# Optimization experiments

Hardware: AMD Instinct MI355X
Metric: run time of the kernel (lower is better)

Reference implementation:

```python
import jax, jax.numpy as jnp
import numpy as np

N = 50000       # nodes
E = 800000      # edges (avg degree 16)
R = 8           # relations
IN = 128        # in_channels
H = 128         # hidden_size
B = 10          # graphs in batch
NPG = N // B    # nodes per graph (equal-size graphs)
NEG_SLOPE = 0.2 # RGATConv default negative_slope


def setup_inputs() -> dict:
    key = jax.random.key(0)
    ks = jax.random.split(key, 12)
    s = 0.1
    x = jax.random.normal(ks[0], (N, IN), dtype=jnp.float32)
    edge_index = jax.random.randint(ks[1], (2, E), 0, N, dtype=jnp.int32)
    edge_type = jax.random.randint(ks[2], (E,), 0, R, dtype=jnp.int32)
    batch = jnp.repeat(jnp.arange(B, dtype=jnp.int32), NPG)
    W1 = jax.random.normal(ks[3], (R, IN, H), dtype=jnp.float32) * s
    q1 = jax.random.normal(ks[4], (H, 1), dtype=jnp.float32) * s
    k1 = jax.random.normal(ks[5], (H, 1), dtype=jnp.float32) * s
    b1 = jnp.zeros((H,), dtype=jnp.float32)
    W2 = jax.random.normal(ks[6], (R, H, H), dtype=jnp.float32) * s
    q2 = jax.random.normal(ks[7], (H, 1), dtype=jnp.float32) * s
    k2 = jax.random.normal(ks[8], (H, 1), dtype=jnp.float32) * s
    b2 = jnp.zeros((H,), dtype=jnp.float32)
    Wl = jax.random.normal(ks[9], (H, H), dtype=jnp.float32) * s
    bl = jnp.zeros((H,), dtype=jnp.float32)
    return dict(x=x, edge_index=edge_index, edge_type=edge_type, batch=batch,
                W1=W1, q1=q1, k1=k1, b1=b1, W2=W2, q2=q2, k2=k2, b2=b2,
                Wl=Wl, bl=bl)


def _rgat_conv(x, src, tgt, etype, W, q, k, b):
    # Per-relation transform once per node ([R,N,H]), then gather per edge;
    # mathematically identical to PyG's per-edge bmm but avoids the [E,in,H] blowup.
    xW = jnp.einsum('ni,rio->rno', x, W)          # [R, N, H]
    outi = xW[etype, tgt]                          # [E, H] transformed target feats
    outj = xW[etype, src]                          # [E, H] transformed source feats
    # additive self-attention, heads=1, dim=1
    alpha = jax.nn.leaky_relu(outi @ q + outj @ k, NEG_SLOPE)  # [E, 1]
    # across-relation segment softmax over incoming edges of each target node
    m = jax.ops.segment_max(alpha, tgt, num_segments=N)        # [N, 1]
    a = jnp.exp(alpha - m[tgt])
    den = jax.ops.segment_sum(a, tgt, num_segments=N)          # [N, 1]
    a = a / (den[tgt] + 1e-16)
    out = jax.ops.segment_sum(a * outj, tgt, num_segments=N)   # [N, H]
    return out + b


def reference(x, edge_index, edge_type, batch, W1, q1, k1, b1,
              W2, q2, k2, b2, Wl, bl):
    src, tgt = edge_index[0], edge_index[1]
    h = jax.nn.relu(_rgat_conv(x, src, tgt, edge_type, W1, q1, k1, b1))
    # dropout p=0 -> identity
    h = jax.nn.relu(_rgat_conv(h, src, tgt, edge_type, W2, q2, k2, b2))
    h = h @ Wl.T + bl                               # nn.Linear
    # to_dense_batch: batch is sorted with equal-size graphs of NPG nodes
    return h.reshape(B, NPG, H)
```

## Files before the change

### kernel.cpp

```cpp
#include <hip/hip_runtime.h>


typedef unsigned int uint;
typedef unsigned short ushort_t;

using bf16x8 = __attribute__((ext_vector_type(8))) __bf16;
using f32x4  = __attribute__((ext_vector_type(4))) float;

__device__ __forceinline__ ushort_t fToBf(float f) {
  uint u = __float_as_uint(f);
  u += 0x7FFFu + ((u >> 16) & 1);
  return (ushort_t)(u >> 16);
}
__device__ __forceinline__ float bfToF(ushort_t h) {
  return __uint_as_float(((uint)h) << 16);
}
__device__ __forceinline__ uint packBf(float a, float b) {
  return (uint)fToBf(a) | ((uint)fToBf(b) << 16);
}


__global__ void k_count(const int* __restrict__ tgt, int* __restrict__ deg, int E) {
  int e = blockIdx.x * 256 + threadIdx.x;
  if (e < E) atomicAdd(&deg[tgt[e]], 1);
}

__global__ void k_scanA(const int* __restrict__ deg, int* __restrict__ incl,
                        int* __restrict__ bsum, int n) {
  __shared__ int s[256];
  int tid = threadIdx.x;
  int i = blockIdx.x * 256 + tid;
  int v = (i < n) ? deg[i] : 0;
  s[tid] = v;
  __syncthreads();
  for (int off = 1; off < 256; off <<= 1) {
    int t = (tid >= off) ? s[tid - off] : 0;
    __syncthreads();
    s[tid] += t;
    __syncthreads();
  }
  if (i < n) incl[i] = s[tid];
  if (tid == 255) bsum[blockIdx.x] = s[255];
}

__global__ void k_scanB(int* __restrict__ bsum, int nb) {
  __shared__ int s[256];
  int tid = threadIdx.x;
  int v = (tid < nb) ? bsum[tid] : 0;
  s[tid] = v;
  __syncthreads();
  for (int off = 1; off < 256; off <<= 1) {
    int t = (tid >= off) ? s[tid - off] : 0;
    __syncthreads();
    s[tid] += t;
    __syncthreads();
  }
  if (tid < nb) bsum[tid] = s[tid] - v;
}

__global__ void k_scanC(const int* __restrict__ deg, const int* __restrict__ incl,
                        const int* __restrict__ bsum, int* __restrict__ rowptr,
                        int n, int E) {
  int i = blockIdx.x * 256 + threadIdx.x;
  if (i < n) {
    rowptr[i] = bsum[blockIdx.x] + incl[i] - deg[i];
    if (i == n - 1) rowptr[n] = E;
  }
}

__global__ void k_scatter(const int* __restrict__ src, const int* __restrict__ tgt,
                          const int* __restrict__ et, const int* __restrict__ rowptr,
                          int* __restrict__ cursor, int* __restrict__ sorted, int E) {
  int e = blockIdx.x * 256 + threadIdx.x;
  if (e >= E) return;
  int t = tgt[e];
  int pos = atomicAdd(&cursor[t], 1);
  sorted[rowptr[t] + pos] = src[e] | (et[e] << 16);
}


__global__ void k_wTf(const float* __restrict__ W1, const float* __restrict__ W2,
                      ushort_t* __restrict__ WTf) {
  int b = blockIdx.x * 4 + (threadIdx.x >> 6);
  int lane = threadIdx.x & 63;
  int layer = b >> 8;
  int r = (b >> 5) & 7;
  int f = b & 31;
  int mt = f >> 2, kb = f & 3;
  const float* W = layer ? W2 : W1;
  int col = mt * 16 + (lane & 15);
  int krow = kb * 32 + (lane >> 4) * 8;
  ushort_t* dst = WTf + ((size_t)b * 64 + lane) * 8;
  #pragma unroll
  for (int j = 0; j < 8; j++)
    dst[j] = fToBf(W[((size_t)r * 128 + krow + j) * 128 + col]);
}

__global__ void k_wqwk(const float* __restrict__ W1, const float* __restrict__ q1,
                       const float* __restrict__ k1, const float* __restrict__ W2,
                       const float* __restrict__ q2, const float* __restrict__ k2,
                       ushort_t* __restrict__ wqk) {
  int g = blockIdx.x * 256 + threadIdx.x;
  if (g >= 4096) return;
  int layer = g >> 11;
  int which = (g >> 10) & 1;
  int idx = g & 1023;
  const float* w = (layer ? W2 : W1) + (size_t)idx * 128;
  const float* v = layer ? (which ? k2 : q2) : (which ? k1 : q1);
  float s = 0.f;
  #pragma unroll 8
  for (int h = 0; h < 128; h++) s += w[h] * v[h];
  int r = idx >> 7, kin = idx & 127;
  wqk[(size_t)layer * 2048 + ((which << 3) + r) * 128 + kin] = fToBf(s);
}


template <bool F32IN>
__global__ __launch_bounds__(256, 2) void
k_xw(const void* __restrict__ Ain,
     const ushort_t* __restrict__ WTf,
     const ushort_t* __restrict__ Wqk,
     ushort_t* __restrict__ xW,
     float* __restrict__ stbl,
     int M) {
  __shared__ __align__(16) ushort_t wbuf[2][16384];
  int tid = threadIdx.x, wv = tid >> 6, lane = tid & 63;
  int l15 = lane & 15, quad = lane >> 4;
  int node0 = blockIdx.x * 128 + wv * 32;

  bf16x8 bx[2][4];
  #pragma unroll
  for (int tile = 0; tile < 2; tile++) {
    int node = node0 + tile * 16 + l15;
    int nc = node < M ? node : M - 1;
    if (F32IN) {
      const float* row = (const float*)Ain + (size_t)nc * 128;
      #pragma unroll
      for (int kb = 0; kb < 4; kb++) {
        float4 a = *(const float4*)(row + kb * 32 + quad * 8);
        float4 b = *(const float4*)(row + kb * 32 + quad * 8 + 4);
        union { bf16x8 v; ushort_t u[8]; } t;
        t.u[0] = fToBf(a.x); t.u[1] = fToBf(a.y); t.u[2] = fToBf(a.z); t.u[3] = fToBf(a.w);
        t.u[4] = fToBf(b.x); t.u[5] = fToBf(b.y); t.u[6] = fToBf(b.z); t.u[7] = fToBf(b.w);
        bx[tile][kb] = t.v;
      }
    } else {
      const ushort_t* row = (const ushort_t*)Ain + (size_t)nc * 128;
      #pragma unroll
      for (int kb = 0; kb < 4; kb++)
        bx[tile][kb] = *(const bf16x8*)(row + kb * 32 + quad * 8);
    }
  }

  #pragma unroll
  for (int i = 0; i < 8; i++)
    *(int4*)(wbuf[0] + (size_t)(tid + i * 256) * 8) =
        *(const int4*)(WTf + (size_t)(tid + i * 256) * 8);
  __syncthreads();

  for (int r = 0; r < 8; r++) {
    int4 pf[8];
    if (r < 7) {
      const ushort_t* src = WTf + (size_t)(r + 1) * 16384;
      #pragma unroll
      for (int i = 0; i < 8; i++)
        pf[i] = *(const int4*)(src + (size_t)(tid + i * 256) * 8);
    }
    const ushort_t* wb = wbuf[r & 1];
    uint2 po[2][8];
    #pragma unroll
    for (int mt = 0; mt < 8; mt++) {
      f32x4 a0 = {}, a1 = {};
      #pragma unroll
      for (int kb = 0; kb < 4; kb++) {
        bf16x8 af = *(const bf16x8*)(wb + (size_t)((mt * 4 + kb) * 64 + lane) * 8);
        a0 = __builtin_amdgcn_mfma_f32_16x16x32_bf16(af, bx[0][kb], a0, 0, 0, 0);
        a1 = __builtin_amdgcn_mfma_f32_16x16x32_bf16(af, bx[1][kb], a1, 0, 0, 0);
      }
      po[0][mt].x = packBf(a0[0], a0[1]); po[0][mt].y = packBf(a0[2], a0[3]);
      po[1][mt].x = packBf(a1[0], a1[1]); po[1][mt].y = packBf(a1[2], a1[3]);
    }
    #pragma unroll
    for (int tile = 0; tile < 2; tile++) {
      int node = node0 + tile * 16 + l15;
      if (node < M) {
        ushort_t* rowp = xW + ((size_t)r * M + node) * 128 + quad * 32;
        #pragma unroll
        for (int i = 0; i < 4; i++) {
          int4 v = {(int)po[tile][2 * i].x, (int)po[tile][2 * i].y,
                    (int)po[tile][2 * i + 1].x, (int)po[tile][2 * i + 1].y};
          *(int4*)(rowp + i * 8) = v;
        }
      }
    }
    if (r < 7) {
      ushort_t* db = wbuf[(r + 1) & 1];
      #pragma unroll
      for (int i = 0; i < 8; i++)
        *(int4*)(db + (size_t)(tid + i * 256) * 8) = pf[i];
    }
    __syncthreads();
  }

  bf16x8 aq[4];
  #pragma unroll
  for (int kb = 0; kb < 4; kb++)
    aq[kb] = *(const bf16x8*)(Wqk + (size_t)l15 * 128 + kb * 32 + quad * 8);
  #pragma unroll
  for (int tile = 0; tile < 2; tile++) {
    f32x4 s = {};
    #pragma unroll
    for (int kb = 0; kb < 4; kb++)
      s = __builtin_amdgcn_mfma_f32_16x16x32_bf16(aq[kb], bx[tile][kb], s, 0, 0, 0);
    int node = node0 + tile * 16 + l15;
    if (node < M) {
      float4 v = {s[0], s[1], s[2], s[3]};
      *(float4*)(stbl + (size_t)node * 16 + quad * 4) = v;
    }
  }
}


#define ACC8(W_, V_)                                                     \
  acc[0] += W_ * bfToF((ushort_t)(V_.x & 0xFFFF));                       \
  acc[1] += W_ * bfToF((ushort_t)(V_.x >> 16));                          \
  acc[2] += W_ * bfToF((ushort_t)(V_.y & 0xFFFF));                       \
  acc[3] += W_ * bfToF((ushort_t)(V_.y >> 16));                          \
  acc[4] += W_ * bfToF((ushort_t)(V_.z & 0xFFFF));                       \
  acc[5] += W_ * bfToF((ushort_t)(V_.z >> 16));                          \
  acc[6] += W_ * bfToF((ushort_t)(V_.w & 0xFFFF));                       \
  acc[7] += W_ * bfToF((ushort_t)(V_.w >> 16));

__global__ __launch_bounds__(256) void
k_aggr(const ushort_t* __restrict__ feat,
       const float* __restrict__ stbl,
       const int* __restrict__ rowptr, const int* __restrict__ sorted,
       const float* __restrict__ bias, ushort_t* __restrict__ outp, int n) {
  int tid = threadIdx.x, wv = tid >> 6, lane = tid & 63;
  int t = blockIdx.x * 4 + wv;
  if (t >= n) return;
  int e0 = rowptr[t], e1 = rowptr[t + 1];
  int g4 = lane >> 4, fcol = lane & 15;

  float m = -INFINITY, den = 0.f;
  float acc[8] = {};

  for (int base = e0; base < e1; base += 64) {
    int cnt = min(64, e1 - base);
    float alpha = -INFINITY;
    int pk = 0;
    if (lane < cnt) {
      pk = sorted[base + lane];
      int s = pk & 0xFFFF, r = pk >> 16;
      float a = stbl[(size_t)t * 16 + r] + stbl[(size_t)s * 16 + 8 + r];
      alpha = (a >= 0.f) ? a : 0.2f * a;
    }
    float cm = alpha;
    #pragma unroll
    for (int off = 32; off; off >>= 1) cm = fmaxf(cm, __shfl_xor(cm, off, 64));
    float nm = fmaxf(m, cm);
    float sc = __expf(m - nm);
    den *= sc;
    #pragma unroll
    for (int i = 0; i < 8; i++) acc[i] *= sc;
    float w = (lane < cnt) ? __expf(alpha - nm) : 0.f;
    float ws = w;
    #pragma unroll
    for (int off = 32; off; off >>= 1) ws += __shfl_xor(ws, off, 64);
    den += ws;
    m = nm;

    for (int g = 0; g < cnt; g += 16) {
      int i0 = g + g4;
      float w0 = __shfl(w, i0, 64);
      float w1 = __shfl(w, i0 + 4, 64);
      float w2 = __shfl(w, i0 + 8, 64);
      float w3 = __shfl(w, i0 + 12, 64);
      int p0 = __shfl(pk, i0, 64);
      int p1 = __shfl(pk, i0 + 4, 64);
      int p2 = __shfl(pk, i0 + 8, 64);
      int p3 = __shfl(pk, i0 + 12, 64);
      const uint4* r0 = (const uint4*)(feat + (size_t)((p0 >> 16) * n + (p0 & 0xFFFF)) * 128) + fcol;
      const uint4* r1 = (const uint4*)(feat + (size_t)((p1 >> 16) * n + (p1 & 0xFFFF)) * 128) + fcol;
      const uint4* r2 = (const uint4*)(feat + (size_t)((p2 >> 16) * n + (p2 & 0xFFFF)) * 128) + fcol;
      const uint4* r3 = (const uint4*)(feat + (size_t)((p3 >> 16) * n + (p3 & 0xFFFF)) * 128) + fcol;
      uint4 v0 = *r0;
      uint4 v1 = *r1;
      uint4 v2 = *r2;
      uint4 v3 = *r3;
      ACC8(w0, v0)
      ACC8(w1, v1)
      ACC8(w2, v2)
      ACC8(w3, v3)
    }
  }

  #pragma unroll
  for (int i = 0; i < 8; i++) acc[i] += __shfl_xor(acc[i], 16, 64);
  #pragma unroll
  for (int i = 0; i < 8; i++) acc[i] += __shfl_xor(acc[i], 32, 64);

  float inv = (den > 0.f) ? 1.f / (den + 1e-16f) : 0.f;
  int base0 = (fcol & 3) * 32 + (fcol >> 2) * 4;
  float4 ba = *(const float4*)(bias + base0);
  float4 bb = *(const float4*)(bias + base0 + 16);
  uint2 oa, ob;
  oa.x = packBf(fmaxf(acc[0] * inv + ba.x, 0.f), fmaxf(acc[1] * inv + ba.y, 0.f));
  oa.y = packBf(fmaxf(acc[2] * inv + ba.z, 0.f), fmaxf(acc[3] * inv + ba.w, 0.f));
  ob.x = packBf(fmaxf(acc[4] * inv + bb.x, 0.f), fmaxf(acc[5] * inv + bb.y, 0.f));
  ob.y = packBf(fmaxf(acc[6] * inv + bb.z, 0.f), fmaxf(acc[7] * inv + bb.w, 0.f));
  if (lane < 16) {
    *(uint2*)(outp + (size_t)t * 128 + base0) = oa;
    *(uint2*)(outp + (size_t)t * 128 + base0 + 16) = ob;
  }
}


#define LDA 136

__global__ __launch_bounds__(256) void
k_gemmL(const ushort_t* __restrict__ A, const float* __restrict__ Wl,
        float* __restrict__ Cout, const float* __restrict__ bias, int M) {
  __shared__ ushort_t As[64 * LDA];
  __shared__ ushort_t Bs[128 * LDA];
  int tid = threadIdx.x;
  int row0 = blockIdx.x * 64;
  for (int c = tid; c < 1024; c += 256) {
    int r = c >> 4, off = (c & 15) * 8;
    int4 v = {0, 0, 0, 0};
    if (row0 + r < M) v = *(const int4*)(A + (size_t)(row0 + r) * 128 + off);
    *(int4*)(As + r * LDA + off) = v;
  }
  for (int c = tid; c < 2048; c += 256) {
    int nn = c >> 4, off = (c & 15) * 8;
    float4 a = *(const float4*)(Wl + (size_t)nn * 128 + off);
    float4 b = *(const float4*)(Wl + (size_t)nn * 128 + off + 4);
    ushort_t* d = Bs + nn * LDA + off;
    d[0] = fToBf(a.x); d[1] = fToBf(a.y); d[2] = fToBf(a.z); d[3] = fToBf(a.w);
    d[4] = fToBf(b.x); d[5] = fToBf(b.y); d[6] = fToBf(b.z); d[7] = fToBf(b.w);
  }
  __syncthreads();
  int wv = tid >> 6, lane = tid & 63;
  int l15 = lane & 15, quad = lane >> 4;
  int wr = wv * 16;
  bf16x8 afr[4];
  #pragma unroll
  for (int kb = 0; kb < 4; kb++)
    afr[kb] = *reinterpret_cast<const bf16x8*>(As + (wr + l15) * LDA + kb * 32 + quad * 8);
  f32x4 acc[8] = {};
  #pragma unroll
  for (int ct = 0; ct < 8; ct++)
    #pragma unroll
    for (int kb = 0; kb < 4; kb++) {
      bf16x8 bfr = *reinterpret_cast<const bf16x8*>(Bs + (ct * 16 + l15) * LDA + kb * 32 + quad * 8);
      acc[ct] = __builtin_amdgcn_mfma_f32_16x16x32_bf16(afr[kb], bfr, acc[ct], 0, 0, 0);
    }
  #pragma unroll
  for (int ct = 0; ct < 8; ct++)
    #pragma unroll
    for (int reg = 0; reg < 4; reg++) {
      int rr = row0 + wr + quad * 4 + reg;
      if (rr < M) Cout[(size_t)rr * 128 + ct * 16 + l15] = acc[ct][reg] + bias[ct * 16 + l15];
    }
}


extern "C" void kernel_launch(void* const* d_in, const int* in_sizes, int n_in,
                              void* d_out, int out_size, void* d_ws, size_t ws_size,
                              hipStream_t stream) {
  const float* x   = (const float*)d_in[0];
  const int* ei    = (const int*)d_in[1];
  const int* etype = (const int*)d_in[2];
  const float* W1  = (const float*)d_in[4];
  const float* q1  = (const float*)d_in[5];
  const float* k1  = (const float*)d_in[6];
  const float* b1  = (const float*)d_in[7];
  const float* W2  = (const float*)d_in[8];
  const float* q2  = (const float*)d_in[9];
  const float* k2  = (const float*)d_in[10];
  const float* b2  = (const float*)d_in[11];
  const float* Wl  = (const float*)d_in[12];
  const float* bl  = (const float*)d_in[13];
  float* out       = (float*)d_out;

  const int N = in_sizes[0] / 128;
  const int E = in_sizes[2];

  char* ws = (char*)d_ws;
  size_t off = 0;
  auto alloc = [&](size_t bytes) {
    size_t o = off;
    off = (off + bytes + 255) & ~(size_t)255;
    return o;
  };

  ushort_t* xW    = (ushort_t*)(ws + alloc((size_t)8 * N * 128 * 2));
  ushort_t* h1    = (ushort_t*)(ws + alloc((size_t)N * 128 * 2));
  ushort_t* h2    = (ushort_t*)(ws + alloc((size_t)N * 128 * 2));
  ushort_t* WTf   = (ushort_t*)(ws + alloc((size_t)2 * 8 * 16384 * 2));
  ushort_t* wqk   = (ushort_t*)(ws + alloc(2 * 16 * 128 * 2));
  float* stblA    = (float*)(ws + alloc((size_t)N * 16 * 4));
  float* stblB    = (float*)(ws + alloc((size_t)N * 16 * 4));
  int* deg        = (int*)(ws + alloc((size_t)N * 4));
  int* cursor     = (int*)(ws + alloc((size_t)N * 4));
  int* incl       = (int*)(ws + alloc((size_t)N * 4));
  int* rowptr     = (int*)(ws + alloc((size_t)(N + 1) * 4));
  int* bsum       = (int*)(ws + alloc(256 * 4));
  int* sorted     = (int*)(ws + alloc((size_t)E * 4));
  (void)ws_size; (void)n_in; (void)out_size;

  const int* srcp = ei;
  const int* tgtp = ei + E;

  int gE = (E + 255) / 256;
  int gN = (N + 255) / 256;
  int gW = (N + 3) / 4;
  int gX = (N + 127) / 128;
  int gL = (N + 63) / 64;

  hipMemsetAsync(deg, 0, (size_t)N * 4, stream);
  hipMemsetAsync(cursor, 0, (size_t)N * 4, stream);
  k_count<<<gE, 256, 0, stream>>>(tgtp, deg, E);
  k_scanA<<<gN, 256, 0, stream>>>(deg, incl, bsum, N);
  k_scanB<<<1, 256, 0, stream>>>(bsum, gN);
  k_scanC<<<gN, 256, 0, stream>>>(deg, incl, bsum, rowptr, N, E);
  k_scatter<<<gE, 256, 0, stream>>>(srcp, tgtp, etype, rowptr, cursor, sorted, E);

  k_wTf<<<128, 256, 0, stream>>>(W1, W2, WTf);
  k_wqwk<<<16, 256, 0, stream>>>(W1, q1, k1, W2, q2, k2, wqk);

  k_xw<true><<<gX, 256, 0, stream>>>(x, WTf, wqk, xW, stblA, N);
  k_aggr<<<gW, 256, 0, stream>>>(xW, stblA, rowptr, sorted, b1, h1, N);

  k_xw<false><<<gX, 256, 0, stream>>>(h1, WTf + (size_t)8 * 16384,
                                      wqk + 2048, xW, stblB, N);
  k_aggr<<<gW, 256, 0, stream>>>(xW, stblB, rowptr, sorted, b2, h2, N);

  k_gemmL<<<gL, 256, 0, stream>>>(h2, Wl, out, bl, N);
}
```

Before: 401.5 us.

## Merge setup kernels, fold block-prefix scan, and shrink xw tile to 64 nodes

Merges the weight-transform, wq/wk precompute and degree zeroing into one launch, replacing two memsets and two kernels. It also folds the block-sum scan into scanC, where each block reduces the preceding block sums itself and initializes the cursor directly to rowptr. The scatter then drops the rowptr lookup. k_xw now processes 64 nodes per block with a single LDS weight buffer instead of 128 nodes double-buffered, trading less weight reuse per block and an extra barrier for more blocks and lower LDS use.

```diff
diff --git a/kernel.cpp b/kernel.cpp
--- a/kernel.cpp
+++ b/kernel.cpp
@@ -43,118 +43,113 @@
   if (tid == 255) bsum[blockIdx.x] = s[255];
 }
 
-__global__ void k_scanB(int* __restrict__ bsum, int nb) {
+__global__ void k_scanC(const int* __restrict__ deg, const int* __restrict__ incl,
+                        const int* __restrict__ bsum, int* __restrict__ rowptr,
+                        int* __restrict__ cursor, int n, int E, int nb) {
   __shared__ int s[256];
   int tid = threadIdx.x;
-  int v = (tid < nb) ? bsum[tid] : 0;
-  s[tid] = v;
+  s[tid] = (tid < nb && tid < (int)blockIdx.x) ? bsum[tid] : 0;
   __syncthreads();
-  for (int off = 1; off < 256; off <<= 1) {
-    int t = (tid >= off) ? s[tid - off] : 0;
+  #pragma unroll
+  for (int off = 128; off; off >>= 1) {
+    if (tid < off) s[tid] += s[tid + off];
     __syncthreads();
-    s[tid] += t;
-    __syncthreads();
-  }
-  if (tid < nb) bsum[tid] = s[tid] - v;
-}
-
-__global__ void k_scanC(const int* __restrict__ deg, const int* __restrict__ incl,
-                        const int* __restrict__ bsum, int* __restrict__ rowptr,
-                        int n, int E) {
-  int i = blockIdx.x * 256 + threadIdx.x;
+  }
+  int prefix = s[0];
+  int i = blockIdx.x * 256 + tid;
   if (i < n) {
-    rowptr[i] = bsum[blockIdx.x] + incl[i] - deg[i];
+    int rp = prefix + incl[i] - deg[i];
+    rowptr[i] = rp;
+    cursor[i] = rp;
     if (i == n - 1) rowptr[n] = E;
   }
 }
 
 __global__ void k_scatter(const int* __restrict__ src, const int* __restrict__ tgt,
-                          const int* __restrict__ et, const int* __restrict__ rowptr,
-                          int* __restrict__ cursor, int* __restrict__ sorted, int E) {
+                          const int* __restrict__ et, int* __restrict__ cursor,
+                          int* __restrict__ sorted, int E) {
   int e = blockIdx.x * 256 + threadIdx.x;
   if (e >= E) return;
-  int t = tgt[e];
-  int pos = atomicAdd(&cursor[t], 1);
-  sorted[rowptr[t] + pos] = src[e] | (et[e] << 16);
-}
-
-
-__global__ void k_wTf(const float* __restrict__ W1, const float* __restrict__ W2,
-                      ushort_t* __restrict__ WTf) {
-  int b = blockIdx.x * 4 + (threadIdx.x >> 6);
-  int lane = threadIdx.x & 63;
-  int layer = b >> 8;
-  int r = (b >> 5) & 7;
-  int f = b & 31;
-  int mt = f >> 2, kb = f & 3;
-  const float* W = layer ? W2 : W1;
-  int col = mt * 16 + (lane & 15);
-  int krow = kb * 32 + (lane >> 4) * 8;
-  ushort_t* dst = WTf + ((size_t)b * 64 + lane) * 8;
-  #pragma unroll
-  for (int j = 0; j < 8; j++)
-    dst[j] = fToBf(W[((size_t)r * 128 + krow + j) * 128 + col]);
-}
-
-__global__ void k_wqwk(const float* __restrict__ W1, const float* __restrict__ q1,
-                       const float* __restrict__ k1, const float* __restrict__ W2,
-                       const float* __restrict__ q2, const float* __restrict__ k2,
-                       ushort_t* __restrict__ wqk) {
-  int g = blockIdx.x * 256 + threadIdx.x;
-  if (g >= 4096) return;
-  int layer = g >> 11;
-  int which = (g >> 10) & 1;
-  int idx = g & 1023;
-  const float* w = (layer ? W2 : W1) + (size_t)idx * 128;
-  const float* v = layer ? (which ? k2 : q2) : (which ? k1 : q1);
-  float s = 0.f;
-  #pragma unroll 8
-  for (int h = 0; h < 128; h++) s += w[h] * v[h];
-  int r = idx >> 7, kin = idx & 127;
-  wqk[(size_t)layer * 2048 + ((which << 3) + r) * 128 + kin] = fToBf(s);
+  int pos = atomicAdd(&cursor[tgt[e]], 1);
+  sorted[pos] = src[e] | (et[e] << 16);
+}
+
+
+__global__ void k_wprep(const float* __restrict__ W1, const float* __restrict__ q1,
+                        const float* __restrict__ k1, const float* __restrict__ W2,
+                        const float* __restrict__ q2, const float* __restrict__ k2,
+                        ushort_t* __restrict__ WTf, ushort_t* __restrict__ wqk,
+                        int* __restrict__ deg, int n) {
+  int blk = blockIdx.x;
+  if (blk < 128) {
+    int b = blk * 4 + (threadIdx.x >> 6);
+    int lane = threadIdx.x & 63;
+    int layer = b >> 8;
+    int r = (b >> 5) & 7;
+    int f = b & 31;
+    int mt = f >> 2, kb = f & 3;
+    const float* W = layer ? W2 : W1;
+    int col = mt * 16 + (lane & 15);
+    int krow = kb * 32 + (lane >> 4) * 8;
+    ushort_t* dst = WTf + ((size_t)b * 64 + lane) * 8;
+    #pragma unroll
+    for (int j = 0; j < 8; j++)
+      dst[j] = fToBf(W[((size_t)r * 128 + krow + j) * 128 + col]);
+  } else if (blk < 144) {
+    int g = (blk - 128) * 256 + threadIdx.x;
+    int layer = g >> 11;
+    int which = (g >> 10) & 1;
+    int idx = g & 1023;
+    const float* w = (layer ? W2 : W1) + (size_t)idx * 128;
+    const float* v = layer ? (which ? k2 : q2) : (which ? k1 : q1);
+    float s = 0.f;
+    #pragma unroll 8
+    for (int h = 0; h < 128; h++) s += w[h] * v[h];
+    int r = idx >> 7, kin = idx & 127;
+    wqk[(size_t)layer * 2048 + ((which << 3) + r) * 128 + kin] = fToBf(s);
+  } else {
+    for (int i = (blk - 144) * 256 + threadIdx.x; i < n; i += 8 * 256)
+      deg[i] = 0;
+  }
 }
 
 
 template <bool F32IN>
-__global__ __launch_bounds__(256, 2) void
+__global__ __launch_bounds__(256) void
 k_xw(const void* __restrict__ Ain,
      const ushort_t* __restrict__ WTf,
      const ushort_t* __restrict__ Wqk,
      ushort_t* __restrict__ xW,
      float* __restrict__ stbl,
      int M) {
-  __shared__ __align__(16) ushort_t wbuf[2][16384];
+  __shared__ __align__(16) ushort_t wbuf[16384];
   int tid = threadIdx.x, wv = tid >> 6, lane = tid & 63;
   int l15 = lane & 15, quad = lane >> 4;
-  int node0 = blockIdx.x * 128 + wv * 32;
-
-  bf16x8 bx[2][4];
-  #pragma unroll
-  for (int tile = 0; tile < 2; tile++) {
-    int node = node0 + tile * 16 + l15;
-    int nc = node < M ? node : M - 1;
-    if (F32IN) {
-      const float* row = (const float*)Ain + (size_t)nc * 128;
-      #pragma unroll
-      for (int kb = 0; kb < 4; kb++) {
-        float4 a = *(const float4*)(row + kb * 32 + quad * 8);
-        float4 b = *(const float4*)(row + kb * 32 + quad * 8 + 4);
-        union { bf16x8 v; ushort_t u[8]; } t;
-        t.u[0] = fToBf(a.x); t.u[1] = fToBf(a.y); t.u[2] = fToBf(a.z); t.u[3] = fToBf(a.w);
-        t.u[4] = fToBf(b.x); t.u[5] = fToBf(b.y); t.u[6] = fToBf(b.z); t.u[7] = fToBf(b.w);
-        bx[tile][kb] = t.v;
-      }
-    } else {
-      const ushort_t* row = (const ushort_t*)Ain + (size_t)nc * 128;
-      #pragma unroll
-      for (int kb = 0; kb < 4; kb++)
-        bx[tile][kb] = *(const bf16x8*)(row + kb * 32 + quad * 8);
-    }
+  int node = blockIdx.x * 64 + wv * 16 + l15;
+  int nc = node < M ? node : M - 1;
+
+  bf16x8 bx[4];
+  if (F32IN) {
+    const float* row = (const float*)Ain + (size_t)nc * 128;
+    #pragma unroll
+    for (int kb = 0; kb < 4; kb++) {
+      float4 a = *(const float4*)(row + kb * 32 + quad * 8);
+      float4 b = *(const float4*)(row + kb * 32 + quad * 8 + 4);
+      union { bf16x8 v; ushort_t u[8]; } t;
+      t.u[0] = fToBf(a.x); t.u[1] = fToBf(a.y); t.u[2] = fToBf(a.z); t.u[3] = fToBf(a.w);
+      t.u[4] = fToBf(b.x); t.u[5] = fToBf(b.y); t.u[6] = fToBf(b.z); t.u[7] = fToBf(b.w);
+      bx[kb] = t.v;
+    }
+  } else {
+    const ushort_t* row = (const ushort_t*)Ain + (size_t)nc * 128;
+    #pragma unroll
+    for (int kb = 0; kb < 4; kb++)
+      bx[kb] = *(const bf16x8*)(row + kb * 32 + quad * 8);
   }
 
   #pragma unroll
   for (int i = 0; i < 8; i++)
-    *(int4*)(wbuf[0] + (size_t)(tid + i * 256) * 8) =
+    *(int4*)(wbuf + (size_t)(tid + i * 256) * 8) =
         *(const int4*)(WTf + (size_t)(tid + i * 256) * 8);
   __syncthreads();
 
@@ -166,57 +161,47 @@
       for (int i = 0; i < 8; i++)
         pf[i] = *(const int4*)(src + (size_t)(tid + i * 256) * 8);
     }
-    const ushort_t* wb = wbuf[r & 1];
-    uint2 po[2][8];
+    uint2 po[8];
     #pragma unroll
     for (int mt = 0; mt < 8; mt++) {
-      f32x4 a0 = {}, a1 = {};
+      f32x4 a = {};
       #pragma unroll
       for (int kb = 0; kb < 4; kb++) {
-        bf16x8 af = *(const bf16x8*)(wb + (size_t)((mt * 4 + kb) * 64 + lane) * 8);
-        a0 = __builtin_amdgcn_mfma_f32_16x16x32_bf16(af, bx[0][kb], a0, 0, 0, 0);
-        a1 = __builtin_amdgcn_mfma_f32_16x16x32_bf16(af, bx[1][kb], a1, 0, 0, 0);
+        bf16x8 af = *(const bf16x8*)(wbuf + (size_t)((mt * 4 + kb) * 64 + lane) * 8);
+        a = __builtin_amdgcn_mfma_f32_16x16x32_bf16(af, bx[kb], a, 0, 0, 0);
       }
-      po[0][mt].x = packBf(a0[0], a0[1]); po[0][mt].y = packBf(a0[2], a0[3]);
-      po[1][mt].x = packBf(a1[0], a1[1]); po[1][mt].y = packBf(a1[2], a1[3]);
-    }
-    #pragma unroll
-    for (int tile = 0; tile < 2; tile++) {
-      int node = node0 + tile * 16 + l15;
-      if (node < M) {
-        ushort_t* rowp = xW + ((size_t)r * M + node) * 128 + quad * 32;
-        #pragma unroll
-        for (int i = 0; i < 4; i++) {
-          int4 v = {(int)po[tile][2 * i].x, (int)po[tile][2 * i].y,
-                    (int)po[tile][2 * i + 1].x, (int)po[tile][2 * i + 1].y};
-          *(int4*)(rowp + i * 8) = v;
-        }
+      po[mt].x = packBf(a[0], a[1]);
+      po[mt].y = packBf(a[2], a[3]);
+    }
+    if (node < M) {
+      ushort_t* rowp = xW + ((size_t)r * M + node) * 128 + quad * 32;
+      #pragma unroll
+      for (int i = 0; i < 4; i++) {
+        int4 v = {(int)po[2 * i].x, (int)po[2 * i].y,
+                  (int)po[2 * i + 1].x, (int)po[2 * i + 1].y};
+        *(int4*)(rowp + i * 8) = v;
       }
     }
     if (r < 7) {
-      ushort_t* db = wbuf[(r + 1) & 1];
+      __syncthreads();
       #pragma unroll
       for (int i = 0; i < 8; i++)
-        *(int4*)(db + (size_t)(tid + i * 256) * 8) = pf[i];
-    }
-    __syncthreads();
+        *(int4*)(wbuf + (size_t)(tid + i * 256) * 8) = pf[i];
+      __syncthreads();
+    }
   }
 
   bf16x8 aq[4];
   #pragma unroll
   for (int kb = 0; kb < 4; kb++)
     aq[kb] = *(const bf16x8*)(Wqk + (size_t)l15 * 128 + kb * 32 + quad * 8);
-  #pragma unroll
-  for (int tile = 0; tile < 2; tile++) {
-    f32x4 s = {};
-    #pragma unroll
-    for (int kb = 0; kb < 4; kb++)
-      s = __builtin_amdgcn_mfma_f32_16x16x32_bf16(aq[kb], bx[tile][kb], s, 0, 0, 0);
-    int node = node0 + tile * 16 + l15;
-    if (node < M) {
-      float4 v = {s[0], s[1], s[2], s[3]};
-      *(float4*)(stbl + (size_t)node * 16 + quad * 4) = v;
-    }
+  f32x4 s = {};
+  #pragma unroll
+  for (int kb = 0; kb < 4; kb++)
+    s = __builtin_amdgcn_mfma_f32_16x16x32_bf16(aq[kb], bx[kb], s, 0, 0, 0);
+  if (node < M) {
+    float4 v = {s[0], s[1], s[2], s[3]};
+    *(float4*)(stbl + (size_t)node * 16 + quad * 4) = v;
   }
 }
 
@@ -415,19 +400,15 @@
   int gE = (E + 255) / 256;
   int gN = (N + 255) / 256;
   int gW = (N + 3) / 4;
-  int gX = (N + 127) / 128;
+  int gX = (N + 63) / 64;
   int gL = (N + 63) / 64;
 
-  hipMemsetAsync(deg, 0, (size_t)N * 4, stream);
-  hipMemsetAsync(cursor, 0, (size_t)N * 4, stream);
+  k_wprep<<<152, 256, 0, stream>>>(W1, q1, k1, W2, q2, k2, WTf, wqk, deg, N);
+
   k_count<<<gE, 256, 0, stream>>>(tgtp, deg, E);
   k_scanA<<<gN, 256, 0, stream>>>(deg, incl, bsum, N);
-  k_scanB<<<1, 256, 0, stream>>>(bsum, gN);
-  k_scanC<<<gN, 256, 0, stream>>>(deg, incl, bsum, rowptr, N, E);
-  k_scatter<<<gE, 256, 0, stream>>>(srcp, tgtp, etype, rowptr, cursor, sorted, E);
-
-  k_wTf<<<128, 256, 0, stream>>>(W1, W2, WTf);
-  k_wqwk<<<16, 256, 0, stream>>>(W1, q1, k1, W2, q2, k2, wqk);
+  k_scanC<<<gN, 256, 0, stream>>>(deg, incl, bsum, rowptr, cursor, N, E, gN);
+  k_scatter<<<gE, 256, 0, stream>>>(srcp, tgtp, etype, cursor, sorted, E);
 
   k_xw<true><<<gX, 256, 0, stream>>>(x, WTf, wqk, xW, stblA, N);
   k_aggr<<<gW, 256, 0, stream>>>(xW, stblA, rowptr, sorted, b1, h1, N);
```

Measured after the change: 497.3 us. 23.8% more time.
